# Optimization experiments

Hardware: AMD Instinct MI355X
Metric: run time of the kernel (lower is better)

## Reference

```python
import jax, jax.numpy as jnp
import numpy as np

B, L, D = 4, 1024, 1024
H, DK, DV = 16, 64, 64
HID = 4 * D
EPS = 1e-5


def layer_norm(x, w, b):
    m = x.mean(-1, keepdims=True)
    v = ((x - m) ** 2).mean(-1, keepdims=True)
    return (x - m) * jax.lax.rsqrt(v + EPS) * w + b


def sln(hl, w, ln_w, ln_b, gamma, beta):
    # Self-modulated LayerNorm: gamma * w * LN(hl) + beta * w
    return gamma * w * layer_norm(hl, ln_w, ln_b) + beta * w


def setup_inputs() -> dict:
    key = jax.random.key(0)
    ks = jax.random.split(key, 20)
    s = 0.02
    inp = {
        "q": jax.random.normal(ks[0], (B, L, D), jnp.float32),
        "k": jax.random.normal(ks[1], (B, L, D), jnp.float32),
        "v": jax.random.normal(ks[2], (B, L, D), jnp.float32),
        "z": jax.random.normal(ks[3], (B, L, D), jnp.float32),
        # projections stored [in, out] (torch Linear applies x @ W.T + b)
        "wq_w": jax.random.normal(ks[4], (D, H * DK), jnp.float32) * s,
        "wq_b": jnp.zeros((H * DK,), jnp.float32),
        "wk_w": jax.random.normal(ks[5], (D, H * DK), jnp.float32) * s,
        "wk_b": jnp.zeros((H * DK,), jnp.float32),
        "wv_w": jax.random.normal(ks[6], (D, H * DV), jnp.float32) * s,
        "wv_b": jnp.zeros((H * DV,), jnp.float32),
        "fc_w": jax.random.normal(ks[7], (H * DV, D), jnp.float32) * s,
        "fc_b": jnp.zeros((D,), jnp.float32),
        "mlp1_w": jax.random.normal(ks[8], (D, HID), jnp.float32) * s,
        "mlp1_b": jnp.zeros((HID,), jnp.float32),
        "mlp2_w": jax.random.normal(ks[9], (HID, D), jnp.float32) * s,
        "mlp2_b": jnp.zeros((D,), jnp.float32),
        "ln1_w": jnp.ones((D,), jnp.float32),
        "ln1_b": jnp.zeros((D,), jnp.float32),
        "g1": jax.random.normal(ks[10], (1, 1, 1), jnp.float32),
        "b1": jax.random.normal(ks[11], (1, 1, 1), jnp.float32),
        "ln2_w": jnp.ones((D,), jnp.float32),
        "ln2_b": jnp.zeros((D,), jnp.float32),
        "g2": jax.random.normal(ks[12], (1, 1, 1), jnp.float32),
        "b2": jax.random.normal(ks[13], (1, 1, 1), jnp.float32),
    }
    return inp


def reference(q, k, v, z,
              wq_w, wq_b, wk_w, wk_b, wv_w, wv_b, fc_w, fc_b,
              mlp1_w, mlp1_b, mlp2_w, mlp2_b,
              ln1_w, ln1_b, g1, b1, ln2_w, ln2_b, g2, b2):
    scale = 1.0 / np.sqrt(DK).astype(np.float32)
    q = sln(q, z, ln1_w, ln1_b, g1, b1)
    residual = q
    qh = (q @ wq_w + wq_b).reshape(B, L, H, DK)
    kh = (k @ wk_w + wk_b).reshape(B, L, H, DK)
    vh = (v @ wv_w + wv_b).reshape(B, L, H, DV)
    # scores per (head, batch) matching torch layout (n_head*sz_b, Lq, Lk)
    attn = jnp.einsum("bqhd,bkhd->hbqk", qh, kh) * scale
    attn = jax.nn.softmax(attn, axis=-1)
    out = jnp.einsum("hbqk,bkhd->bqhd", attn, vh).reshape(B, L, H * DV)
    out = out @ fc_w + fc_b
    out = out + residual
    h = sln(out, z, ln2_w, ln2_b, g2, b2)
    h = jax.nn.gelu(h @ mlp1_w + mlp1_b, approximate=False)
    out = (h @ mlp2_w + mlp2_b) + out
    return out, attn.reshape(H * B, L, L)
```

## Files before the change

kernel.cpp:

```cpp
#include <hip/hip_runtime.h>
#include <math.h>

namespace {

constexpr int kL  = 1024;
constexpr int kD  = 1024;
constexpr int kB  = 4;
constexpr int kH  = 16;
constexpr int kDK = 64;
constexpr int kHID = 4096;

typedef unsigned short ushort_t;
typedef short  s16x8 __attribute__((ext_vector_type(8)));
typedef float  f32x4 __attribute__((ext_vector_type(4)));
typedef unsigned short u16x4 __attribute__((ext_vector_type(4)));

__device__ __forceinline__ ushort_t f2bf(float f) {
    unsigned u = __float_as_uint(f);
    unsigned r = u + 0x7fffu + ((u >> 16) & 1u);
    return (ushort_t)(r >> 16);
}

__device__ __forceinline__ void gld16(const void* g, void* l) {
    __builtin_amdgcn_global_load_lds((__attribute__((address_space(1))) void*)(g),
                                     (__attribute__((address_space(3))) void*)(l),
                                     16, 0, 0);
}

__device__ __forceinline__ float wred_sum(float v) {
    #pragma unroll
    for (int o = 32; o > 0; o >>= 1) v += __shfl_xor(v, o, 64);
    return v;
}

__global__ __launch_bounds__(256) void sln_kernel(
    const float* __restrict__ x, const float* __restrict__ z,
    const float* __restrict__ lnw, const float* __restrict__ lnb,
    const float* __restrict__ g, const float* __restrict__ bt,
    float* __restrict__ outf, ushort_t* __restrict__ outb)
{
    const int row = blockIdx.x;
    const int tid = threadIdx.x;
    const size_t base = (size_t)row * kD;
    float4 xv = ((const float4*)(x + base))[tid];
    float s  = xv.x + xv.y + xv.z + xv.w;
    float sq = xv.x * xv.x + xv.y * xv.y + xv.z * xv.z + xv.w * xv.w;
    __shared__ float r1[4], r2[4];
    float ws = wred_sum(s), wq = wred_sum(sq);
    int lane = tid & 63, wid = tid >> 6;
    if (lane == 0) { r1[wid] = ws; r2[wid] = wq; }
    __syncthreads();
    float st = r1[0] + r1[1] + r1[2] + r1[3];
    float qt = r2[0] + r2[1] + r2[2] + r2[3];
    float mean = st * (1.0f / kD);
    float var  = qt * (1.0f / kD) - mean * mean;
    float rs = rsqrtf(var + 1e-5f);
    float gv = g[0], bv = bt[0];
    float4 zv = ((const float4*)(z + base))[tid];
    float4 wv = ((const float4*)lnw)[tid];
    float4 lb = ((const float4*)lnb)[tid];
    float4 o;
    o.x = zv.x * (gv * ((xv.x - mean) * rs * wv.x + lb.x) + bv);
    o.y = zv.y * (gv * ((xv.y - mean) * rs * wv.y + lb.y) + bv);
    o.z = zv.z * (gv * ((xv.z - mean) * rs * wv.z + lb.z) + bv);
    o.w = zv.w * (gv * ((xv.w - mean) * rs * wv.w + lb.w) + bv);
    if (outf) ((float4*)(outf + base))[tid] = o;
    u16x4 ob; ob[0] = f2bf(o.x); ob[1] = f2bf(o.y); ob[2] = f2bf(o.z); ob[3] = f2bf(o.w);
    ((u16x4*)(outb + base))[tid] = ob;
}

__global__ __launch_bounds__(256) void cvt_bf16(
    const float* __restrict__ x, ushort_t* __restrict__ y)
{
    int i = blockIdx.x * 256 + threadIdx.x;
    f32x4 v = ((const f32x4*)x)[i];
    u16x4 o; o[0] = f2bf(v[0]); o[1] = f2bf(v[1]); o[2] = f2bf(v[2]); o[3] = f2bf(v[3]);
    ((u16x4*)y)[i] = o;
}

__global__ __launch_bounds__(256) void twcvt(
    const float* __restrict__ src, ushort_t* __restrict__ dst, int R, int C)
{
    __shared__ float t[32][33];
    int c0 = blockIdx.x * 32, r0 = blockIdx.y * 32;
    int tx = threadIdx.x & 31, ty = threadIdx.x >> 5;
    #pragma unroll
    for (int i = 0; i < 4; i++) {
        int r = ty + i * 8;
        t[r][tx] = src[(size_t)(r0 + r) * C + c0 + tx];
    }
    __syncthreads();
    #pragma unroll
    for (int i = 0; i < 4; i++) {
        int c = ty + i * 8;
        dst[(size_t)(c0 + c) * R + r0 + tx] = f2bf(t[tx][c]);
    }
}

__global__ __launch_bounds__(256) void vtrans(
    const ushort_t* __restrict__ vh, ushort_t* __restrict__ vhT)
{
    __shared__ ushort_t t[32][33];
    int p = blockIdx.z, b = p & 3, h = p >> 2;
    int j0 = blockIdx.x * 32, d0 = blockIdx.y * 32;
    int tx = threadIdx.x & 31, ty = threadIdx.x >> 5;
    const ushort_t* src = vh + (size_t)b * (kL * kD) + h * kDK;
    #pragma unroll
    for (int i = 0; i < 4; i++) {
        int j = ty + i * 8;
        t[j][tx] = src[(size_t)(j0 + j) * kD + d0 + tx];
    }
    __syncthreads();
    ushort_t* dst = vhT + (size_t)p * (kDK * kL);
    #pragma unroll
    for (int i = 0; i < 4; i++) {
        int d = ty + i * 8;
        dst[(size_t)(d0 + d) * kL + j0 + tx] = t[tx][d];
    }
}

__global__ __launch_bounds__(256) void mgemm(
    const ushort_t* __restrict__ A, int lda,
    const ushort_t* __restrict__ Bt, int ldb,
    void* __restrict__ Cv, int ldc, int K,
    const float* __restrict__ bias, const float* __restrict__ res,
    float scale, int flags, int mode,
    const float* __restrict__ bias1, const float* __restrict__ bias2)
{
    __shared__ __align__(16) ushort_t As[128 * 32];
    __shared__ __align__(16) ushort_t Bs[128 * 32];
    float*    Cf = (float*)Cv;
    ushort_t* Cb = (ushort_t*)Cv;
    if (mode == 2) {
        int z = blockIdx.z;
        A  += (size_t)z * (4096u * 1024u);
        Bt += (size_t)z * (1024u * 1024u);
        Cb += (size_t)z * (4096u * 1024u);
        if (z == 1) bias = bias1;
        else if (z == 2) bias = bias2;
    }
    const int tid = threadIdx.x;
    const int lane = tid & 63, w = tid >> 6;
    const int m0 = blockIdx.y * 128, n0 = blockIdx.x * 128;
    const int r0 = tid >> 2;
    const int c0 = (tid & 3) ^ (r0 & 3);
    const ushort_t* Ag0 = A  + (size_t)(m0 + r0) * lda + c0 * 8;
    const ushort_t* Ag1 = Ag0 + (size_t)64 * lda;
    const ushort_t* Bg0 = Bt + (size_t)(n0 + r0) * ldb + c0 * 8;
    const ushort_t* Bg1 = Bg0 + (size_t)64 * ldb;
    char* AsW = (char*)As + w * 1024;
    char* BsW = (char*)Bs + w * 1024;
    const int wm = (w & 1) * 64, wn = (w >> 1) * 64;
    const int fn = lane & 15, q = lane >> 4;
    int aoff[4], boff[4];
    #pragma unroll
    for (int i = 0; i < 4; i++) {
        int ra = wm + i * 16 + fn;
        aoff[i] = (ra * 4 + (q ^ (ra & 3))) * 16;
        int rb = wn + i * 16 + fn;
        boff[i] = (rb * 4 + (q ^ (rb & 3))) * 16;
    }
    f32x4 acc[4][4] = {};
    for (int k0 = 0; k0 < K; k0 += 32) {
        gld16(Ag0 + k0, AsW);
        gld16(Ag1 + k0, AsW + 4096);
        gld16(Bg0 + k0, BsW);
        gld16(Bg1 + k0, BsW + 4096);
        __syncthreads();
        s16x8 af[4], bfr[4];
        #pragma unroll
        for (int i = 0; i < 4; i++) {
            af[i]  = *(const s16x8*)((const char*)As + aoff[i]);
            bfr[i] = *(const s16x8*)((const char*)Bs + boff[i]);
        }
        #pragma unroll
        for (int mi = 0; mi < 4; mi++)
            #pragma unroll
            for (int ni = 0; ni < 4; ni++)
                acc[mi][ni] = __builtin_amdgcn_mfma_f32_16x16x32_bf16(
                    af[mi], bfr[ni], acc[mi][ni], 0, 0, 0);
        __syncthreads();
    }
    #pragma unroll
    for (int mi = 0; mi < 4; mi++) {
        #pragma unroll
        for (int ni = 0; ni < 4; ni++) {
            #pragma unroll
            for (int r = 0; r < 4; r++) {
                int gm = m0 + wm + mi * 16 + q * 4 + r;
                int gn = n0 + wn + ni * 16 + fn;
                float v = acc[mi][ni][r] * scale;
                if (bias) v += bias[gn];
                if (flags & 1) v = 0.5f * v * (1.0f + erff(v * 0.70710678118654752f));
                if (res) v += res[(size_t)gm * ldc + gn];
                if (flags & 2) Cb[(size_t)gm * ldc + gn] = f2bf(v);
                else           Cf[(size_t)gm * ldc + gn] = v;
            }
        }
    }
}

__global__ __launch_bounds__(512) void fused_attn(
    const ushort_t* __restrict__ qh, const ushort_t* __restrict__ kh,
    const ushort_t* __restrict__ vhT, float* __restrict__ attn,
    ushort_t* __restrict__ ctx)
{
    __shared__ float redm[8][32];
    __shared__ float reds[8][32];
    __shared__ float cred[4][2048];
    const int p = blockIdx.y, b = p & 3, h = p >> 2;
    const int m0 = blockIdx.x * 32;
    const int tid = threadIdx.x;
    const int lane = tid & 63, w = tid >> 6;
    const int fn = lane & 15, q = lane >> 4;
    const ushort_t* Qb = qh + (size_t)b * (kL * kD) + h * 64;
    const ushort_t* Kb = kh + (size_t)b * (kL * kD) + h * 64;
    float* Pp = attn + (size_t)p * kL * kL;

    f32x4 acc[2][8] = {};
    #pragma unroll
    for (int kk = 0; kk < 2; kk++) {
        s16x8 aq[2], bq[8];
        #pragma unroll
        for (int mi = 0; mi < 2; mi++)
            aq[mi] = *(const s16x8*)(Qb + (size_t)(m0 + mi * 16 + fn) * kD + kk * 32 + q * 8);
        #pragma unroll
        for (int ni = 0; ni < 8; ni++)
            bq[ni] = *(const s16x8*)(Kb + (size_t)(w * 128 + ni * 16 + fn) * kD + kk * 32 + q * 8);
        #pragma unroll
        for (int mi = 0; mi < 2; mi++)
            #pragma unroll
            for (int ni = 0; ni < 8; ni++)
                acc[mi][ni] = __builtin_amdgcn_mfma_f32_16x16x32_bf16(
                    aq[mi], bq[ni], acc[mi][ni], 0, 0, 0);
    }

    float mloc[2][4];
    #pragma unroll
    for (int mi = 0; mi < 2; mi++) {
        #pragma unroll
        for (int r = 0; r < 4; r++) {
            float m = -3.0e38f;
            #pragma unroll
            for (int ni = 0; ni < 8; ni++) {
                acc[mi][ni][r] *= 0.125f;
                m = fmaxf(m, acc[mi][ni][r]);
            }
            mloc[mi][r] = m;
        }
    }
    #pragma unroll
    for (int o = 1; o < 16; o <<= 1) {
        #pragma unroll
        for (int mi = 0; mi < 2; mi++)
            #pragma unroll
            for (int r = 0; r < 4; r++)
                mloc[mi][r] = fmaxf(mloc[mi][r], __shfl_xor(mloc[mi][r], o, 64));
    }
    if (fn == 0) {
        #pragma unroll
        for (int mi = 0; mi < 2; mi++)
            #pragma unroll
            for (int r = 0; r < 4; r++)
                redm[w][mi * 16 + q * 4 + r] = mloc[mi][r];
    }
    __syncthreads();
    #pragma unroll
    for (int mi = 0; mi < 2; mi++) {
        #pragma unroll
        for (int r = 0; r < 4; r++) {
            int row = mi * 16 + q * 4 + r;
            float m = redm[0][row];
            #pragma unroll
            for (int w2 = 1; w2 < 8; w2++) m = fmaxf(m, redm[w2][row]);
            float s = 0.f;
            #pragma unroll
            for (int ni = 0; ni < 8; ni++) {
                float e = __expf(acc[mi][ni][r] - m);
                acc[mi][ni][r] = e;
                s += e;
            }
            mloc[mi][r] = s;
        }
    }
    #pragma unroll
    for (int o = 1; o < 16; o <<= 1) {
        #pragma unroll
        for (int mi = 0; mi < 2; mi++)
            #pragma unroll
            for (int r = 0; r < 4; r++)
                mloc[mi][r] += __shfl_xor(mloc[mi][r], o, 64);
    }
    if (fn == 0) {
        #pragma unroll
        for (int mi = 0; mi < 2; mi++)
            #pragma unroll
            for (int r = 0; r < 4; r++)
                reds[w][mi * 16 + q * 4 + r] = mloc[mi][r];
    }
    __syncthreads();
    float inv[2][4];
    #pragma unroll
    for (int mi = 0; mi < 2; mi++) {
        #pragma unroll
        for (int r = 0; r < 4; r++) {
            int row = mi * 16 + q * 4 + r;
            float s = reds[0][row];
            #pragma unroll
            for (int w2 = 1; w2 < 8; w2++) s += reds[w2][row];
            inv[mi][r] = 1.0f / s;
        }
    }
    #pragma unroll
    for (int mi = 0; mi < 2; mi++)
        #pragma unroll
        for (int ni = 0; ni < 8; ni++)
            #pragma unroll
            for (int r = 0; r < 4; r++)
                Pp[(size_t)(m0 + mi * 16 + q * 4 + r) * kL + w * 128 + ni * 16 + fn]
                    = acc[mi][ni][r] * inv[mi][r];
    __syncthreads();

    const ushort_t* Vb = vhT + (size_t)p * (kDK * kL);
    f32x4 acc2[2][4] = {};
    #pragma unroll
    for (int kk = 0; kk < 4; kk++) {
        s16x8 pa[2];
        #pragma unroll
        for (int mi = 0; mi < 2; mi++) {
            const float* src = Pp + (size_t)(m0 + mi * 16 + fn) * kL + w * 128 + kk * 32 + q * 8;
            f32x4 v0 = *(const f32x4*)src;
            f32x4 v1 = *(const f32x4*)(src + 4);
            s16x8 t;
            t[0] = (short)f2bf(v0[0]); t[1] = (short)f2bf(v0[1]);
            t[2] = (short)f2bf(v0[2]); t[3] = (short)f2bf(v0[3]);
            t[4] = (short)f2bf(v1[0]); t[5] = (short)f2bf(v1[1]);
            t[6] = (short)f2bf(v1[2]); t[7] = (short)f2bf(v1[3]);
            pa[mi] = t;
        }
        #pragma unroll
        for (int nj = 0; nj < 4; nj++) {
            s16x8 bv = *(const s16x8*)(Vb + (size_t)(nj * 16 + fn) * kL + w * 128 + kk * 32 + q * 8);
            #pragma unroll
            for (int mi = 0; mi < 2; mi++)
                acc2[mi][nj] = __builtin_amdgcn_mfma_f32_16x16x32_bf16(
                    pa[mi], bv, acc2[mi][nj], 0, 0, 0);
        }
    }
    if (w < 4) {
        #pragma unroll
        for (int mi = 0; mi < 2; mi++)
            #pragma unroll
            for (int nj = 0; nj < 4; nj++)
                #pragma unroll
                for (int r = 0; r < 4; r++)
                    cred[w][(mi * 16 + q * 4 + r) * 64 + nj * 16 + fn] = acc2[mi][nj][r];
    }
    __syncthreads();
    if (w >= 4) {
        #pragma unroll
        for (int mi = 0; mi < 2; mi++)
            #pragma unroll
            for (int nj = 0; nj < 4; nj++)
                #pragma unroll
                for (int r = 0; r < 4; r++)
                    cred[w - 4][(mi * 16 + q * 4 + r) * 64 + nj * 16 + fn] += acc2[mi][nj][r];
    }
    __syncthreads();
    {
        int idx0 = tid * 4;
        int row = idx0 >> 6, d0 = idx0 & 63;
        f32x4 s0 = *(const f32x4*)&cred[0][idx0];
        #pragma unroll
        for (int wb = 1; wb < 4; wb++) {
            f32x4 t = *(const f32x4*)&cred[wb][idx0];
            s0[0] += t[0]; s0[1] += t[1]; s0[2] += t[2]; s0[3] += t[3];
        }
        u16x4 o;
        o[0] = f2bf(s0[0]); o[1] = f2bf(s0[1]); o[2] = f2bf(s0[2]); o[3] = f2bf(s0[3]);
        *(u16x4*)(ctx + (size_t)b * (kL * kD) + (size_t)(m0 + row) * kD + h * 64 + d0) = o;
    }
}

}

extern "C" void kernel_launch(void* const* d_in, const int* in_sizes, int n_in,
                              void* d_out, int out_size, void* d_ws, size_t ws_size,
                              hipStream_t stream)
{
    (void)in_sizes; (void)n_in; (void)out_size; (void)ws_size;
    const float* q      = (const float*)d_in[0];
    const float* k      = (const float*)d_in[1];
    const float* v      = (const float*)d_in[2];
    const float* z      = (const float*)d_in[3];
    const float* wq_w   = (const float*)d_in[4];
    const float* wq_b   = (const float*)d_in[5];
    const float* wk_w   = (const float*)d_in[6];
    const float* wk_b   = (const float*)d_in[7];
    const float* wv_w   = (const float*)d_in[8];
    const float* wv_b   = (const float*)d_in[9];
    const float* fc_w   = (const float*)d_in[10];
    const float* fc_b   = (const float*)d_in[11];
    const float* mlp1_w = (const float*)d_in[12];
    const float* mlp1_b = (const float*)d_in[13];
    const float* mlp2_w = (const float*)d_in[14];
    const float* mlp2_b = (const float*)d_in[15];
    const float* ln1_w  = (const float*)d_in[16];
    const float* ln1_b  = (const float*)d_in[17];
    const float* g1     = (const float*)d_in[18];
    const float* b1     = (const float*)d_in[19];
    const float* ln2_w  = (const float*)d_in[20];
    const float* ln2_b  = (const float*)d_in[21];
    const float* g2     = (const float*)d_in[22];
    const float* b2     = (const float*)d_in[23];

    float* out0 = (float*)d_out;
    float* attn = (float*)d_out + (size_t)kB * kL * kD;

    char* arena = (char*)d_ws;
    const size_t MB = 1u << 20;
    float*    qp   = (float*)(arena);
    ushort_t* qh   = (ushort_t*)(arena + 16 * MB);
    ushort_t* kh   = (ushort_t*)(arena + 24 * MB);
    ushort_t* vh   = (ushort_t*)(arena + 32 * MB);
    ushort_t* vhT  = (ushort_t*)(arena + 40 * MB);
    ushort_t* hid  = (ushort_t*)(arena + 16 * MB);
    ushort_t* qb   = (ushort_t*)(arena + 48 * MB);
    ushort_t* kb   = (ushort_t*)(arena + 56 * MB);
    float*    out1 = (float*)(arena + 48 * MB);
    ushort_t* vb   = (ushort_t*)(arena + 64 * MB);
    ushort_t* ctx  = (ushort_t*)(arena + 64 * MB);
    ushort_t* h2   = (ushort_t*)(arena + 72 * MB);
    ushort_t* wqT  = (ushort_t*)(arena + 80 * MB);
    ushort_t* wkT  = (ushort_t*)(arena + 82 * MB);
    ushort_t* wvT  = (ushort_t*)(arena + 84 * MB);
    ushort_t* fcT  = (ushort_t*)(arena + 86 * MB);
    ushort_t* m1T  = (ushort_t*)(arena + 88 * MB);
    ushort_t* m2T  = (ushort_t*)(arena + 96 * MB);

    dim3 blk(256);
    twcvt<<<dim3(32, 32), blk, 0, stream>>>(wq_w, wqT, kD, kH * kDK);
    twcvt<<<dim3(32, 32), blk, 0, stream>>>(wk_w, wkT, kD, kH * kDK);
    twcvt<<<dim3(32, 32), blk, 0, stream>>>(wv_w, wvT, kD, kH * kDK);
    twcvt<<<dim3(32, 32), blk, 0, stream>>>(fc_w, fcT, kH * kDK, kD);
    twcvt<<<dim3(128, 32), blk, 0, stream>>>(mlp1_w, m1T, kD, kHID);
    twcvt<<<dim3(32, 128), blk, 0, stream>>>(mlp2_w, m2T, kHID, kD);
    cvt_bf16<<<dim3(4096), blk, 0, stream>>>(k, kb);
    cvt_bf16<<<dim3(4096), blk, 0, stream>>>(v, vb);
    sln_kernel<<<dim3(kB * kL), blk, 0, stream>>>(q, z, ln1_w, ln1_b, g1, b1, qp, qb);
    mgemm<<<dim3(8, 32, 3), blk, 0, stream>>>(qb, kD, wqT, kD, qh, kD, kD,
                                              wq_b, nullptr, 1.0f, 2, 2, wk_b, wv_b);
    vtrans<<<dim3(32, 2, 64), blk, 0, stream>>>(vh, vhT);
    fused_attn<<<dim3(kL / 32, 64), dim3(512), 0, stream>>>(qh, kh, vhT, attn, ctx);
    mgemm<<<dim3(8, 32, 1), blk, 0, stream>>>(ctx, kD, fcT, kD, out1, kD, kD,
                                              fc_b, qp, 1.0f, 0, 0, nullptr, nullptr);
    sln_kernel<<<dim3(kB * kL), blk, 0, stream>>>(out1, z, ln2_w, ln2_b, g2, b2, nullptr, h2);
    mgemm<<<dim3(32, 32, 1), blk, 0, stream>>>(h2, kD, m1T, kD, hid, kHID, kD,
                                               mlp1_b, nullptr, 1.0f, 3, 0, nullptr, nullptr);
    mgemm<<<dim3(8, 32, 1), blk, 0, stream>>>(hid, kHID, m2T, kHID, out0, kD, kHID,
                                              mlp2_b, out1, 1.0f, 0, 0, nullptr, nullptr);
}
```

Measured before the change: 917.3 us.

## Stage attention probabilities in LDS instead of re-reading from global memory

The fused attention kernel no longer reads its normalized probabilities back from global memory for the P·V matmul. Each wave converts its unnormalized scores to bf16 into a swizzled LDS buffer, runs the MFMAs from there, and applies the 1/sum factor to the accumulators afterwards. The global attn write becomes a nontemporal store, and the block index is remapped to change the order in which blocks are scheduled. The LDS buffer is reused for the cross-wave reduction, which saves shared memory. The bf16 rounding now happens before normalization, so numerics change slightly.

```diff
diff --git a/kernel.cpp b/kernel.cpp
--- a/kernel.cpp
+++ b/kernel.cpp
@@ -205,11 +205,13 @@
     const ushort_t* __restrict__ vhT, float* __restrict__ attn,
     ushort_t* __restrict__ ctx)
 {
+    __shared__ __align__(16) char PlBuf[8 * 4096];
     __shared__ float redm[8][32];
     __shared__ float reds[8][32];
-    __shared__ float cred[4][2048];
-    const int p = blockIdx.y, b = p & 3, h = p >> 2;
-    const int m0 = blockIdx.x * 32;
+    const int orig = blockIdx.y * 32 + blockIdx.x;
+    const int nf = (orig & 7) * 256 + (orig >> 3);
+    const int p = nf >> 5, b = p & 3, h = p >> 2;
+    const int m0 = (nf & 31) * 32;
     const int tid = threadIdx.x;
     const int lane = tid & 63, w = tid >> 6;
     const int fn = lane & 15, q = lane >> 4;
@@ -317,36 +319,57 @@
         for (int ni = 0; ni < 8; ni++)
             #pragma unroll
             for (int r = 0; r < 4; r++)
-                Pp[(size_t)(m0 + mi * 16 + q * 4 + r) * kL + w * 128 + ni * 16 + fn]
-                    = acc[mi][ni][r] * inv[mi][r];
-    __syncthreads();
+                __builtin_nontemporal_store(
+                    acc[mi][ni][r] * inv[mi][r],
+                    &Pp[(size_t)(m0 + mi * 16 + q * 4 + r) * kL + w * 128 + ni * 16 + fn]);
 
     const ushort_t* Vb = vhT + (size_t)p * (kDK * kL);
+    char* Plw = PlBuf + w * 4096;
     f32x4 acc2[2][4] = {};
     #pragma unroll
-    for (int kk = 0; kk < 4; kk++) {
-        s16x8 pa[2];
-        #pragma unroll
-        for (int mi = 0; mi < 2; mi++) {
-            const float* src = Pp + (size_t)(m0 + mi * 16 + fn) * kL + w * 128 + kk * 32 + q * 8;
-            f32x4 v0 = *(const f32x4*)src;
-            f32x4 v1 = *(const f32x4*)(src + 4);
-            s16x8 t;
-            t[0] = (short)f2bf(v0[0]); t[1] = (short)f2bf(v0[1]);
-            t[2] = (short)f2bf(v0[2]); t[3] = (short)f2bf(v0[3]);
-            t[4] = (short)f2bf(v1[0]); t[5] = (short)f2bf(v1[1]);
-            t[6] = (short)f2bf(v1[2]); t[7] = (short)f2bf(v1[3]);
-            pa[mi] = t;
-        }
-        #pragma unroll
-        for (int nj = 0; nj < 4; nj++) {
-            s16x8 bv = *(const s16x8*)(Vb + (size_t)(nj * 16 + fn) * kL + w * 128 + kk * 32 + q * 8);
-            #pragma unroll
-            for (int mi = 0; mi < 2; mi++)
-                acc2[mi][nj] = __builtin_amdgcn_mfma_f32_16x16x32_bf16(
-                    pa[mi], bv, acc2[mi][nj], 0, 0, 0);
-        }
-    }
+    for (int half = 0; half < 2; half++) {
+        #pragma unroll
+        for (int mi = 0; mi < 2; mi++)
+            #pragma unroll
+            for (int ni = 0; ni < 4; ni++)
+                #pragma unroll
+                for (int r = 0; r < 4; r++) {
+                    int row = mi * 16 + q * 4 + r;
+                    int cl  = ni * 16 + fn;
+                    *(ushort_t*)(Plw + ((row * 128 + cl * 2) ^ ((row & 7) << 4)))
+                        = f2bf(acc[mi][half * 4 + ni][r]);
+                }
+        #pragma unroll
+        for (int kh = 0; kh < 2; kh++) {
+            int kk = half * 2 + kh;
+            s16x8 pa[2];
+            #pragma unroll
+            for (int mi = 0; mi < 2; mi++) {
+                int row = mi * 16 + fn;
+                pa[mi] = *(const s16x8*)(Plw +
+                    ((row * 128 + (kh * 32 + q * 8) * 2) ^ ((row & 7) << 4)));
+            }
+            #pragma unroll
+            for (int nj = 0; nj < 4; nj++) {
+                s16x8 bv = *(const s16x8*)(Vb + (size_t)(nj * 16 + fn) * kL +
+                                           w * 128 + kk * 32 + q * 8);
+                #pragma unroll
+                for (int mi = 0; mi < 2; mi++)
+                    acc2[mi][nj] = __builtin_amdgcn_mfma_f32_16x16x32_bf16(
+                        pa[mi], bv, acc2[mi][nj], 0, 0, 0);
+            }
+        }
+    }
+    #pragma unroll
+    for (int mi = 0; mi < 2; mi++)
+        #pragma unroll
+        for (int nj = 0; nj < 4; nj++)
+            #pragma unroll
+            for (int r = 0; r < 4; r++)
+                acc2[mi][nj][r] *= inv[mi][r];
+
+    __syncthreads();
+    float (*cred)[2048] = (float (*)[2048])PlBuf;
     if (w < 4) {
         #pragma unroll
         for (int mi = 0; mi < 2; mi++)
```

Result: faster. 824.3 us (-10.1%).
